# Performance work log

Hardware: AMD Instinct MI355X
Metric: run time of the kernel (lower is better)

The kernel has to match this reference:

```python
import jax, jax.numpy as jnp
import numpy as np

H, W = 40, 128
P = H * W            # image tokens
N = P                # point tokens (matches source where N == Hh*Wh)
C = 128
K = 5                # expand_num
PAD = K // 2
KK = K * K           # 25 neighbors
SPOT = 5             # spot_num
NEG = -1e8


def _l2n(x, axis):
    return x / jnp.clip(jnp.linalg.norm(x, axis=axis, keepdims=True), 1e-12)


def _patches(x, mode, cval=0.0):
    # x: (..., H, W) -> (KK, ..., H, W): KxK sliding windows in F.unfold order
    pw = [(0, 0)] * (x.ndim - 2) + [(PAD, PAD), (PAD, PAD)]
    if mode == 'edge':
        xp = jnp.pad(x, pw, mode='edge')
    else:
        xp = jnp.pad(x, pw, mode='constant', constant_values=cval)
    return jnp.stack([xp[..., i:i + H, j:j + W] for i in range(K) for j in range(K)], 0)


def _knn_idx(pts):
    # (N,3) -> (N,KK) nearest-neighbor indices (self first), as knn_points does
    d2 = jnp.sum((pts[:, None, :] - pts[None, :, :]) ** 2, -1)  # (N,N)
    _, idx = jax.lax.top_k(-d2, KK)
    return idx


def setup_inputs():
    key = jax.random.key(0)
    k1, k2, k3 = jax.random.split(key, 3)
    return {
        'im_feats_h': jax.random.normal(k1, (1, P, C), jnp.float32),
        'pc_feats_h': jax.random.normal(k2, (1, N, C), jnp.float32),
        'points_h': jax.random.normal(k3, (1, N, 3), jnp.float32),
    }


def _forward(imf, pcf, nb):
    # imf: (P,C) image features, pcf: (N,C) point features, nb: (N,KK) point knn
    # --- im_similarity_scores ---
    fmap = imf.T.reshape(C, H, W)
    pat = _patches(fmap, 'edge')                                 # (KK,C,H,W)
    sim = jnp.sum(_l2n(pat, 1) * _l2n(fmap, 0)[None], 1)         # (KK,H,W)
    sim_score = jax.nn.softmax(sim, axis=0)
    # --- pairwise_scores im->pc ---
    s = _l2n(imf, -1) @ _l2n(pcf, -1).T                          # (P,N)
    best_score = s.max(-1).reshape(H, W)
    best_index = s.argmax(-1)                                    # (P,)
    # --- im_select_score ---
    conf = _patches(best_score, 'edge')                          # (KK,H,W)
    idxg = jnp.arange(P).reshape(H, W)
    idx_pat = _patches(idxg, 'const', -1).reshape(KK, P)         # (KK,P)
    select = jnp.where(idx_pat.reshape(KK, H, W) == -1, NEG, sim_score * conf)
    # --- im_seeding ---
    sel = select.at[KK // 2].set(NEG).reshape(KK, P).T           # (P,KK)
    _, tki = jax.lax.top_k(sel, SPOT - 1)
    tki = jnp.concatenate([jnp.full((P, 1), KK // 2, tki.dtype), tki], 1)  # (P,SPOT)
    nb_pix = jnp.clip(jnp.take_along_axis(idx_pat.T, tki, 1), 0, P - 1)
    seed = best_index[nb_pix]                                    # (P,SPOT) pc idx
    # --- im_spoting: expand seeds by point knn, scatter mask, topk-reduce ---
    spot = nb[seed].reshape(P, SPOT * KK)                        # (P,125)
    m = jnp.zeros((P, N), jnp.float32).at[jnp.arange(P)[:, None], spot].set(1.0)
    spot_mask, spot_idx_redu = jax.lax.top_k(m, SPOT * KK)
    # --- pc_similarity_scores ---
    sim_pc = jax.nn.softmax(
        jnp.sum(_l2n(pcf, -1)[:, None] * _l2n(pcf[nb], -1), -1), -1)  # (N,KK)
    # --- pc branch (symmetric, source truncated) ---
    s2 = _l2n(pcf, -1) @ _l2n(imf, -1).T                         # (N,P)
    best_pc_score = s2.max(-1)
    best_pc_idx = s2.argmax(-1)
    select_pc = (sim_pc * best_pc_score[nb]).at[:, 0].set(NEG)   # exclude self
    _, tkp = jax.lax.top_k(select_pc, SPOT - 1)
    tkp = jnp.concatenate([jnp.zeros((N, 1), tkp.dtype), tkp], 1)
    pc_seed = best_pc_idx[jnp.take_along_axis(nb, tkp, 1)]       # (N,SPOT) pixel idx
    # --- pc_spoting: expand seeds in a KxK pixel window ---
    off = jnp.arange(-PAD, PAD + 1)
    r = jnp.clip(pc_seed[..., None, None] // W + off[:, None], 0, H - 1)
    c = jnp.clip(pc_seed[..., None, None] % W + off[None, :], 0, W - 1)
    spot2 = (r * W + c).reshape(N, SPOT * KK)                    # (N,125)
    m2 = jnp.zeros((N, P), jnp.float32).at[jnp.arange(N)[:, None], spot2].set(1.0)
    spot_mask_pc, spot_idx_redu_pc = jax.lax.top_k(m2, SPOT * KK)
    return (select[None], spot_mask[None], spot_idx_redu[None],
            spot_idx_redu_pc[None], spot_mask_pc[None])


def reference(im_feats_h, pc_feats_h, points_h):
    nb = _knn_idx(points_h[0])
    return _forward(im_feats_h[0], pc_feats_h[0], nb)
```

## Files before the change

kernel.cpp:

```cpp
#include <hip/hip_runtime.h>
#include <hip/hip_fp16.h>
#include <float.h>
#include <math.h>

#define HH 40
#define WW 128
#define PP 5120
#define NN 5120
#define CC 128
#define KK 25
#define SPOT 5
#define NEGV -1e8f

#define CSPL 8
#define NSEG 16
#define EPS  1e-4f
#define LOSC 2048.0f
#define RSEGS 16
#define RSEGL (NN / RSEGS)
#define NRMB ((PP + NN) / 4)

typedef _Float16 half8 __attribute__((ext_vector_type(8)));
typedef float f32x4 __attribute__((ext_vector_type(4)));

__global__ __launch_bounds__(256) void k_prep(const float* __restrict__ imf,
                                              const float* __restrict__ pcf,
                                              const float* __restrict__ pts,
                                              float* __restrict__ imn, float* __restrict__ pcn,
                                              __half* __restrict__ imh, __half* __restrict__ iml,
                                              __half* __restrict__ pch, __half* __restrict__ pcl,
                                              int* __restrict__ nb, int* __restrict__ cnt) {
    __shared__ int hist[256];
    __shared__ int wsum2[2][4];
    __shared__ int wsum[4];
    __shared__ int wmin[4];
    __shared__ int s_b, s_need, s_cntLess;
    __shared__ unsigned long long sel[32];
    int t = threadIdx.x;
    int wid = t >> 6, lane = t & 63;

    if (blockIdx.x < NRMB) {
        if (blockIdx.x == 0 && t < 4) cnt[t] = 0;
        int row = blockIdx.x * 4 + wid;
        const float* src; float* dst; __half* dh; __half* dl; int r;
        if (row < PP) { src = imf; dst = imn; dh = imh; dl = iml; r = row; }
        else          { src = pcf; dst = pcn; dh = pch; dl = pcl; r = row - PP; }
        float2 v = *(const float2*)&src[r * CC + lane * 2];
        double ss = (double)v.x * (double)v.x + (double)v.y * (double)v.y;
#pragma unroll
        for (int o = 32; o; o >>= 1) ss += __shfl_xor(ss, o);
        double inv = 1.0 / fmax(sqrt(ss), 1e-12);
        float2 o2 = make_float2((float)((double)v.x * inv), (float)((double)v.y * inv));
        *(float2*)&dst[r * CC + lane * 2] = o2;
        __half hx = __float2half_rn(o2.x), hy = __float2half_rn(o2.y);
        float rx = o2.x - __half2float(hx), ry = o2.y - __half2float(hy);
        __half2 hh; hh.x = hx; hh.y = hy;
        __half2 ll; ll.x = __float2half_rn(rx * LOSC); ll.y = __float2half_rn(ry * LOSC);
        *(__half2*)&dh[r * CC + lane * 2] = hh;
        *(__half2*)&dl[r * CC + lane * 2] = ll;
        return;
    }

    int i = blockIdx.x - NRMB;
    float px = pts[i * 3 + 0], py = pts[i * 3 + 1], pz = pts[i * 3 + 2];

    unsigned k[20];
#pragma unroll
    for (int e = 0; e < 20; ++e) {
        int j = e * 256 + t;
        float dx = __fsub_rn(px, pts[j * 3 + 0]);
        float dy = __fsub_rn(py, pts[j * 3 + 1]);
        float dz = __fsub_rn(pz, pts[j * 3 + 2]);
        float s = __fadd_rn(__fadd_rn(__fmul_rn(dx, dx), __fmul_rn(dy, dy)),
                            __fmul_rn(dz, dz));
        k[e] = __float_as_uint(s);
    }

    int need = KK;
    unsigned bpre = 0;
    for (int bit = 7; bit >= 0; --bit) {
        int c = 0;
        unsigned want = bpre << 1;
#pragma unroll
        for (int e = 0; e < 20; ++e)
            c += ((k[e] >> (24 + bit)) == want);
#pragma unroll
        for (int o = 32; o; o >>= 1) c += __shfl_xor(c, o);
        int par = bit & 1;
        if (lane == 0) wsum2[par][wid] = c;
        __syncthreads();
        int tot = wsum2[par][0] + wsum2[par][1] + wsum2[par][2] + wsum2[par][3];
        if (tot >= need) bpre = want;
        else { bpre = want | 1; need -= tot; }
    }
    unsigned prefix = bpre << 24;

    for (int l = 1; l < 4; ++l) {
        int shift = 24 - 8 * l;
        hist[t] = 0;
        __syncthreads();
        unsigned pmask = 0xFFFFFFFFu << (shift + 8);
#pragma unroll
        for (int e = 0; e < 20; ++e)
            if ((k[e] & pmask) == prefix)
                atomicAdd(&hist[(k[e] >> shift) & 255], 1);
        __syncthreads();
        int v = hist[t], c = v;
#pragma unroll
        for (int o = 1; o < 64; o <<= 1) {
            int u = __shfl_up(c, o);
            if (lane >= o) c += u;
        }
        if (lane == 63) wsum[wid] = c;
        __syncthreads();
        for (int wv = 0; wv < wid; ++wv) c += wsum[wv];
        int cex = c - v;
        if (cex < need && c >= need) { s_b = t; s_need = need - cex; }
        __syncthreads();
        prefix |= ((unsigned)s_b) << shift;
        need = s_need;
        __syncthreads();
    }

    unsigned K = prefix;
    int needK = need;

    if (t == 0) s_cntLess = 0;
    __syncthreads();
#pragma unroll
    for (int e = 0; e < 20; ++e) {
        if (k[e] < K) {
            int slot = atomicAdd(&s_cntLess, 1);
            if (slot < 32)
                sel[slot] = ((unsigned long long)k[e] << 32) | (unsigned)(e * 256 + t);
        }
    }
    __syncthreads();
    int nl = s_cntLess;

    if (t < nl) {
        unsigned long long mine = sel[t];
        int rk = 0;
        for (int s = 0; s < nl; ++s) rk += (sel[s] < mine);
        nb[i * KK + rk] = (int)(mine & 0xFFFFFFFFull);
    }

    unsigned tmask = 0;
#pragma unroll
    for (int e = 0; e < 20; ++e)
        if (k[e] == K) tmask |= 1u << e;

    for (int q = 0; q < needK; ++q) {
        int mi = tmask ? ((__ffs(tmask) - 1) * 256 + t) : 0x7fffffff;
#pragma unroll
        for (int o = 32; o; o >>= 1) mi = min(mi, __shfl_xor(mi, o));
        if (lane == 0) wmin[wid] = mi;
        __syncthreads();
        int g = min(min(wmin[0], wmin[1]), min(wmin[2], wmin[3]));
        if (t == 0) nb[i * KK + nl + q] = g;
        if ((g & 255) == t) tmask &= ~(1u << (g >> 8));
        __syncthreads();
    }
}

__global__ __launch_bounds__(256) void k_rowmax(const __half* __restrict__ imh,
                                                const __half* __restrict__ iml,
                                                const __half* __restrict__ pch,
                                                const __half* __restrict__ pcl,
                                                float* __restrict__ pval,
                                                float* __restrict__ pv2,
                                                int* __restrict__ pidx) {
    const __half* Ah = (blockIdx.z == 0) ? imh : pch;
    const __half* Al = (blockIdx.z == 0) ? iml : pcl;
    const __half* Bh = (blockIdx.z == 0) ? pch : imh;
    const __half* Bl = (blockIdx.z == 0) ? pcl : iml;
    __shared__ char sB[2 * 16384];

    int t = threadIdx.x;
    int wave = t >> 6, l = t & 63;
    int wrow = wave >> 1, wcol = wave & 1;
    int lg = l >> 4, lc = l & 15;
    int rb = blockIdx.x * 64;
    const int segLen = NN / CSPL;
    const int nCh = segLen / 32;
    int segbase = blockIdx.y * segLen;
    int srow = l >> 4;
    int sblk = l & 15;

    half8 Afh[2][4], Afl[2][4];
#pragma unroll
    for (int rt = 0; rt < 2; ++rt)
#pragma unroll
        for (int ks = 0; ks < 4; ++ks) {
            int row = rb + wrow * 32 + rt * 16 + lc;
            int ho = ks * 32 + lg * 8;
            Afh[rt][ks] = *(const half8*)&Ah[(size_t)row * CC + ho];
            Afl[rt][ks] = *(const half8*)&Al[(size_t)row * CC + ho];
        }

    float v1[2][4], v2[2][4]; int i1[2][4];
#pragma unroll
    for (int rt = 0; rt < 2; ++rt)
#pragma unroll
        for (int rg = 0; rg < 4; ++rg) { v1[rt][rg] = -1e30f; v2[rt][rg] = -1e30f; i1[rt][rg] = 0; }

    auto stage = [&](int bufsel, int chbase) {
#pragma unroll
        for (int b = 0; b < 2; ++b) {
            int rbase = wave * 8 + b * 4;
            int r = rbase + srow;
            int gblk = sblk ^ (r & 7);
            __builtin_amdgcn_global_load_lds(
                (const __attribute__((address_space(1))) void*)
                    &Bh[(size_t)(chbase + r) * CC + gblk * 8],
                (__attribute__((address_space(3))) void*)
                    (sB + bufsel * 16384 + rbase * 256),
                16, 0, 0);
            __builtin_amdgcn_global_load_lds(
                (const __attribute__((address_space(1))) void*)
                    &Bl[(size_t)(chbase + r) * CC + gblk * 8],
                (__attribute__((address_space(3))) void*)
                    (sB + bufsel * 16384 + 8192 + rbase * 256),
                16, 0, 0);
        }
    };

    stage(0, segbase);
    __syncthreads();

    int cur = 0;
    for (int c = 0; c < nCh; ++c) {
        if (c + 1 < nCh) stage(cur ^ 1, segbase + (c + 1) * 32);

        f32x4 aH[2], aX[2];
#pragma unroll
        for (int rt = 0; rt < 2; ++rt) {
            aH[rt] = (f32x4){0.f, 0.f, 0.f, 0.f};
            aX[rt] = (f32x4){0.f, 0.f, 0.f, 0.f};
        }

        const char* bufp = sB + cur * 16384;
#pragma unroll
        for (int ks = 0; ks < 4; ++ks) {
            int kb = ks * 64 + lg * 16;
            int row = wcol * 16 + lc;
            int off = row * 256 + (kb ^ ((row & 7) << 4));
            half8 bh = *(const half8*)(bufp + off);
            half8 bl = *(const half8*)(bufp + 8192 + off);
#pragma unroll
            for (int rt = 0; rt < 2; ++rt) {
                aH[rt] = __builtin_amdgcn_mfma_f32_16x16x32_f16(
                    Afh[rt][ks], bh, aH[rt], 0, 0, 0);
                aX[rt] = __builtin_amdgcn_mfma_f32_16x16x32_f16(
                    Afh[rt][ks], bl, aX[rt], 0, 0, 0);
                aX[rt] = __builtin_amdgcn_mfma_f32_16x16x32_f16(
                    Afl[rt][ks], bh, aX[rt], 0, 0, 0);
            }
        }

#pragma unroll
        for (int rt = 0; rt < 2; ++rt) {
            int col = segbase + c * 32 + wcol * 16 + lc;
#pragma unroll
            for (int rg = 0; rg < 4; ++rg) {
                float v = aH[rt][rg] + aX[rt][rg] * (1.0f / LOSC);
                bool gt = v > v1[rt][rg];
                v2[rt][rg] = gt ? v1[rt][rg] : fmaxf(v2[rt][rg], v);
                i1[rt][rg] = gt ? col : i1[rt][rg];
                v1[rt][rg] = gt ? v : v1[rt][rg];
            }
        }
        __syncthreads();
        cur ^= 1;
    }

#pragma unroll
    for (int rt = 0; rt < 2; ++rt)
#pragma unroll
        for (int rg = 0; rg < 4; ++rg) {
            float a1 = v1[rt][rg], a2 = v2[rt][rg]; int ai = i1[rt][rg];
#pragma unroll
            for (int o = 1; o < 16; o <<= 1) {
                float o1 = __shfl_xor(a1, o);
                float o2v = __shfl_xor(a2, o);
                int   oi = __shfl_xor(ai, o);
                if (o1 > a1) { a2 = fmaxf(a1, o2v); a1 = o1; ai = oi; }
                else         { a2 = fmaxf(a2, o1); }
            }
            if (lc == 0) {
                int seg = blockIdx.y * 2 + wcol;
                size_t o = ((size_t)blockIdx.z * NSEG + seg) * PP
                         + rb + wrow * 32 + rt * 16 + lg * 4 + rg;
                pval[o] = a1; pv2[o] = a2; pidx[o] = ai;
            }
        }
}

__global__ void k_reduce_exact(const float* __restrict__ pval, const float* __restrict__ pv2,
                               const int* __restrict__ pidx,
                               const float* __restrict__ imn, const float* __restrict__ pcn,
                               int* __restrict__ bestI, int* __restrict__ bestPI,
                               double* __restrict__ bestSd, double* __restrict__ bestPSd,
                               int* __restrict__ list2, int* __restrict__ cnt) {
    int wid = threadIdx.x >> 6, lane = threadIdx.x & 63;
    int row = blockIdx.x * 4 + wid;
    int side = (row >= PP) ? 1 : 0;
    int r = side ? (row - PP) : row;
    size_t base = (size_t)side * NSEG * PP + r;

    float v1 = -1e30f, v2 = -1e30f; int i1 = 0x7fffffff;
    if (lane < NSEG) {
        v1 = pval[base + (size_t)lane * PP];
        v2 = pv2[base + (size_t)lane * PP];
        i1 = pidx[base + (size_t)lane * PP];
    }
#pragma unroll
    for (int o = 1; o < 16; o <<= 1) {
        float o1 = __shfl_xor(v1, o);
        float o2v = __shfl_xor(v2, o);
        int   oi = __shfl_xor(i1, o);
        if (o1 > v1) { v2 = fmaxf(v1, o2v); v1 = o1; i1 = oi; }
        else         { v2 = fmaxf(v2, o1); }
    }
    int bi = __shfl(i1, 0);
    float b1 = __shfl(v1, 0), b2 = __shfl(v2, 0);

    const float* A = side ? pcn : imn;
    const float* B = side ? imn : pcn;
    float2 av = *(const float2*)&A[(size_t)r * CC + lane * 2];
    float2 bv = *(const float2*)&B[(size_t)bi * CC + lane * 2];
    double s = (double)av.x * (double)bv.x + (double)av.y * (double)bv.y;
#pragma unroll
    for (int o = 32; o; o >>= 1) s += __shfl_xor(s, o);

    if (lane == 0) {
        if (side == 0) { bestI[r] = bi; bestSd[r] = s; }
        else           { bestPI[r] = bi; bestPSd[r] = s; }
        if (b1 - b2 < EPS) {
            int slot = atomicAdd(&cnt[0], 1);
            list2[slot] = r | (side << 16);
        }
    }
}

__global__ void k_recheck64a(const float* __restrict__ imn, const float* __restrict__ pcn,
                             const int* __restrict__ list2, const int* __restrict__ cnt,
                             double* __restrict__ rqv, int* __restrict__ rqi) {
    __shared__ double ad[CC];
    __shared__ double rv[4];
    __shared__ int    ri[4];
    int seg = blockIdx.x, t = threadIdx.x;
    int wid = t >> 6, lane = t & 63;
    int total = cnt[0];
    for (int e = blockIdx.y; e < total; e += gridDim.y) {
        __syncthreads();
        int ent = list2[e];
        int r = ent & 0xffff, side = ent >> 16;
        const float* Arow = (side == 0 ? imn : pcn) + (size_t)r * CC;
        const float* B    = (side == 0 ? pcn : imn);
        if (t < CC) ad[t] = (double)Arow[t];
        __syncthreads();
        double bv = -1e300; int bi = 0x7fffffff;
        for (int j = seg * RSEGL + t; j < (seg + 1) * RSEGL; j += 256) {
            double s0 = 0.0, s1 = 0.0, s2 = 0.0, s3 = 0.0;
#pragma unroll 8
            for (int c4 = 0; c4 < CC / 4; ++c4) {
                float4 b = *(const float4*)&B[(size_t)j * CC + c4 * 4];
                s0 += ad[c4 * 4 + 0] * (double)b.x;
                s1 += ad[c4 * 4 + 1] * (double)b.y;
                s2 += ad[c4 * 4 + 2] * (double)b.z;
                s3 += ad[c4 * 4 + 3] * (double)b.w;
            }
            double s = (s0 + s1) + (s2 + s3);
            if (s > bv || (s == bv && j < bi)) { bv = s; bi = j; }
        }
#pragma unroll
        for (int o = 32; o; o >>= 1) {
            double ov = __shfl_xor(bv, o); int oi = __shfl_xor(bi, o);
            if (ov > bv || (ov == bv && oi < bi)) { bv = ov; bi = oi; }
        }
        if (lane == 0) { rv[wid] = bv; ri[wid] = bi; }
        __syncthreads();
        if (t == 0) {
            for (int wv = 1; wv < 4; ++wv)
                if (rv[wv] > bv || (rv[wv] == bv && ri[wv] < bi)) { bv = rv[wv]; bi = ri[wv]; }
            rqv[(size_t)e * RSEGS + seg] = bv;
            rqi[(size_t)e * RSEGS + seg] = bi;
        }
        __syncthreads();
    }
}

__global__ void k_recheck64b(const int* __restrict__ list2, const int* __restrict__ cnt,
                             const double* __restrict__ rqv, const int* __restrict__ rqi,
                             double* __restrict__ bestSd, int* __restrict__ bestI,
                             double* __restrict__ bestPSd, int* __restrict__ bestPI) {
    int e = blockIdx.x * 256 + threadIdx.x;
    if (e >= cnt[0]) return;
    double bv = rqv[(size_t)e * RSEGS]; int bi = rqi[(size_t)e * RSEGS];
#pragma unroll 4
    for (int s = 1; s < RSEGS; ++s) {
        double ov = rqv[(size_t)e * RSEGS + s]; int oi = rqi[(size_t)e * RSEGS + s];
        if (ov > bv || (ov == bv && oi < bi)) { bv = ov; bi = oi; }
    }
    int ent = list2[e];
    int r = ent & 0xffff, side = ent >> 16;
    if (side == 0) { bestSd[r] = bv; bestI[r] = bi; }
    else           { bestPSd[r] = bv; bestPI[r] = bi; }
}

__device__ __forceinline__ void compact_bits_par(const unsigned* bits,
                                                 float* __restrict__ sm,
                                                 float* __restrict__ si, int lane) {
    unsigned w0 = bits[lane];
    unsigned w1 = bits[64 + lane];
    unsigned w2 = (lane < 32) ? bits[128 + lane] : 0u;
    int c0 = __popc(w0), c1 = __popc(w1), c2 = __popc(w2);
    int s0 = c0, s1 = c1, s2 = c2;
#pragma unroll
    for (int o = 1; o < 64; o <<= 1) {
        int u0 = __shfl_up(s0, o); if (lane >= o) s0 += u0;
        int u1 = __shfl_up(s1, o); if (lane >= o) s1 += u1;
        int u2 = __shfl_up(s2, o); if (lane >= o) s2 += u2;
    }
    int tot0 = __shfl(s0, 63);
    int tot1 = __shfl(s1, 63);
    int tot2 = __shfl(s2, 31);
    int nl = tot0 + tot1 + tot2;
    int e0 = s0 - c0;
    int e1 = tot0 + (s1 - c1);
    int e2 = tot0 + tot1 + (s2 - c2);

    {
        int base = e0; unsigned word = w0; int wi = lane;
        while (word) { int pos = __ffs(word) - 1;
            si[base] = (float)(wi * 32 + pos); sm[base] = 1.0f; word &= word - 1; ++base; }
        base = e1; word = w1; wi = 64 + lane;
        while (word) { int pos = __ffs(word) - 1;
            si[base] = (float)(wi * 32 + pos); sm[base] = 1.0f; word &= word - 1; ++base; }
        if (lane < 32) {
            base = e2; word = w2; wi = 128 + lane;
            while (word) { int pos = __ffs(word) - 1;
                si[base] = (float)(wi * 32 + pos); sm[base] = 1.0f; word &= word - 1; ++base; }
        }
    }
    {
        int wi = lane; int base = nl + 32 * wi - e0; unsigned word = ~w0;
        while (word && base < 125) { int pos = __ffs(word) - 1;
            si[base] = (float)(wi * 32 + pos); sm[base] = 0.0f; word &= word - 1; ++base; }
        wi = 64 + lane; base = nl + 32 * wi - e1; word = ~w1;
        while (word && base < 125) { int pos = __ffs(word) - 1;
            si[base] = (float)(wi * 32 + pos); sm[base] = 0.0f; word &= word - 1; ++base; }
        if (lane < 32) {
            wi = 128 + lane; base = nl + 32 * wi - e2; word = ~w2;
            while (word && base < 125) { int pos = __ffs(word) - 1;
                si[base] = (float)(wi * 32 + pos); sm[base] = 0.0f; word &= word - 1; ++base; }
        }
    }
}

__global__ void k_select_spot(const float* __restrict__ imn, const float* __restrict__ pcn,
                              const int* __restrict__ nb,
                              const double* __restrict__ bestSd, const int* __restrict__ bestI,
                              const double* __restrict__ bestPSd, const int* __restrict__ bestPI,
                              float* __restrict__ outSelect,
                              float* __restrict__ outMask, float* __restrict__ outIdx,
                              float* __restrict__ outMaskPc, float* __restrict__ outIdxPc) {
    __shared__ unsigned bits[4][160];
    __shared__ float smv[4][125];
    __shared__ float siv[4][125];
    int t = threadIdx.x;
    int wid = t >> 6, lane = t & 63;
    int bid = blockIdx.x;

    if (bid < PP / 4) {
        int pb = (bid & 7) * (PP / 4 / 8) + (bid >> 3);
        int p = pb * 4 + wid;
        int h = p >> 7, w = p & 127;

        double mysim = -1e300;
        if (lane < KK) {
            int di = lane / 5 - 2, dj = lane % 5 - 2;
            int hc = min(max(h + di, 0), HH - 1);
            int wc = min(max(w + dj, 0), WW - 1);
            const float* crow = &imn[(size_t)p * CC];
            const float* nrow = &imn[(size_t)(hc * WW + wc) * CC];
            double s0 = 0.0, s1 = 0.0, s2 = 0.0, s3 = 0.0;
#pragma unroll 8
            for (int c = 0; c < CC; c += 4) {
                float4 cv = *(const float4*)&crow[c];
                float4 nv = *(const float4*)&nrow[c];
                s0 += (double)cv.x * (double)nv.x;
                s1 += (double)cv.y * (double)nv.y;
                s2 += (double)cv.z * (double)nv.z;
                s3 += (double)cv.w * (double)nv.w;
            }
            mysim = (s0 + s1) + (s2 + s3);
        }
        double mx = mysim;
#pragma unroll
        for (int o = 1; o < 64; o <<= 1) mx = fmax(mx, __shfl_xor(mx, o));

        double e = 0.0;
        if (lane < KK) e = exp(mysim - mx);
        double sum = e;
#pragma unroll
        for (int o = 32; o; o >>= 1) sum += __shfl_xor(sum, o);
        double inv = 1.0 / sum;

        double selv = -1e300;
        if (lane < KK) {
            int di = lane / 5 - 2, dj = lane % 5 - 2;
            int h2 = h + di, w2 = w + dj;
            bool valid = (h2 >= 0 && h2 < HH && w2 >= 0 && w2 < WW);
            int hc = min(max(h2, 0), HH - 1), wc = min(max(w2, 0), WW - 1);
            double conf = bestSd[hc * WW + wc];
            double so = valid ? (e * inv * conf) : (double)NEGV;
            outSelect[lane * PP + p] = (float)so;
            selv = (lane == 12) ? (double)NEGV : so;
        }

        int tks[5]; tks[0] = 12;
        double sv = selv; int sk = (lane < KK) ? lane : 63;
#pragma unroll
        for (int s = 0; s < 4; ++s) {
            double bv = sv; int bk = sk;
#pragma unroll
            for (int o = 1; o < 64; o <<= 1) {
                double ov = __shfl_xor(bv, o);
                int ok = __shfl_xor(bk, o);
                if (ov > bv || (ov == bv && ok < bk)) { bv = ov; bk = ok; }
            }
            tks[s + 1] = bk;
            if (sk == bk) sv = -1e300;
        }

        int sd0, sd1, sd2, sd3, sd4;
#pragma unroll
        for (int s = 0; s < 5; ++s) {
            int k = tks[s];
            int di = k / 5 - 2, dj = k % 5 - 2;
            int h2 = h + di, w2 = w + dj;
            int pix = (h2 >= 0 && h2 < HH && w2 >= 0 && w2 < WW) ? (h2 * WW + w2) : -1;
            pix = min(max(pix, 0), PP - 1);
            int sd = bestI[pix];
            if (s == 0) sd0 = sd; else if (s == 1) sd1 = sd;
            else if (s == 2) sd2 = sd; else if (s == 3) sd3 = sd; else sd4 = sd;
        }

        for (int w2 = lane; w2 < 160; w2 += 64) bits[wid][w2] = 0u;
        __syncthreads();
        for (int e2 = lane; e2 < 125; e2 += 64) {
            int q = e2 / 25;
            int sd = (q == 0) ? sd0 : (q == 1) ? sd1 : (q == 2) ? sd2 : (q == 3) ? sd3 : sd4;
            int pt = nb[sd * KK + (e2 % 25)];
            atomicOr(&bits[wid][pt >> 5], 1u << (pt & 31));
        }
        __syncthreads();
        compact_bits_par(bits[wid], smv[wid], siv[wid], lane);
        for (int e2 = lane; e2 < 125; e2 += 64) {
            outMask[p * 125 + e2] = smv[wid][e2];
            outIdx[p * 125 + e2]  = siv[wid][e2];
        }
    } else {
        int bid2 = bid - PP / 4;
        int ib = (bid2 & 7) * (PP / 4 / 8) + (bid2 >> 3);
        int i = ib * 4 + wid;

        double mysim = -1e300;
        if (lane < KK) {
            int nbs = nb[i * KK + lane];
            const float* crow = &pcn[(size_t)i * CC];
            const float* nrow = &pcn[(size_t)nbs * CC];
            double s0 = 0.0, s1 = 0.0, s2 = 0.0, s3 = 0.0;
#pragma unroll 8
            for (int c = 0; c < CC; c += 4) {
                float4 cv = *(const float4*)&crow[c];
                float4 nv = *(const float4*)&nrow[c];
                s0 += (double)cv.x * (double)nv.x;
                s1 += (double)cv.y * (double)nv.y;
                s2 += (double)cv.z * (double)nv.z;
                s3 += (double)cv.w * (double)nv.w;
            }
            mysim = (s0 + s1) + (s2 + s3);
        }
        double mx = mysim;
#pragma unroll
        for (int o = 1; o < 64; o <<= 1) mx = fmax(mx, __shfl_xor(mx, o));

        double e = 0.0;
        if (lane < KK) e = exp(mysim - mx);
        double sum = e;
#pragma unroll
        for (int o = 32; o; o >>= 1) sum += __shfl_xor(sum, o);
        double inv = 1.0 / sum;

        double selv = -1e300;
        if (lane < KK)
            selv = (lane == 0) ? (double)NEGV : (e * inv * bestPSd[nb[i * KK + lane]]);

        int tks[5]; tks[0] = 0;
        double sv = selv; int sk = (lane < KK) ? lane : 63;
#pragma unroll
        for (int s = 0; s < 4; ++s) {
            double bv = sv; int bk = sk;
#pragma unroll
            for (int o = 1; o < 64; o <<= 1) {
                double ov = __shfl_xor(bv, o);
                int ok = __shfl_xor(bk, o);
                if (ov > bv || (ov == bv && ok < bk)) { bv = ov; bk = ok; }
            }
            tks[s + 1] = bk;
            if (sk == bk) sv = -1e300;
        }

        int sd0, sd1, sd2, sd3, sd4;
#pragma unroll
        for (int s = 0; s < 5; ++s) {
            int nbs = nb[i * KK + tks[s]];
            int sd = bestPI[nbs];
            if (s == 0) sd0 = sd; else if (s == 1) sd1 = sd;
            else if (s == 2) sd2 = sd; else if (s == 3) sd3 = sd; else sd4 = sd;
        }

        for (int w2 = lane; w2 < 160; w2 += 64) bits[wid][w2] = 0u;
        __syncthreads();
        for (int e2 = lane; e2 < 125; e2 += 64) {
            int q = e2 / 25;
            int sd = (q == 0) ? sd0 : (q == 1) ? sd1 : (q == 2) ? sd2 : (q == 3) ? sd3 : sd4;
            int kk = e2 % 25;
            int r0 = sd >> 7, c0 = sd & 127;
            int r = min(max(r0 + kk / 5 - 2, 0), HH - 1);
            int c = min(max(c0 + kk % 5 - 2, 0), WW - 1);
            int pix = r * WW + c;
            atomicOr(&bits[wid][pix >> 5], 1u << (pix & 31));
        }
        __syncthreads();
        compact_bits_par(bits[wid], smv[wid], siv[wid], lane);
        for (int e2 = lane; e2 < 125; e2 += 64) {
            outMaskPc[i * 125 + e2] = smv[wid][e2];
            outIdxPc[i * 125 + e2]  = siv[wid][e2];
        }
    }
}

extern "C" void kernel_launch(void* const* d_in, const int* in_sizes, int n_in,
                              void* d_out, int out_size, void* d_ws, size_t ws_size,
                              hipStream_t stream) {
    const float* imf = (const float*)d_in[0];
    const float* pcf = (const float*)d_in[1];
    const float* pts = (const float*)d_in[2];
    float* out = (float*)d_out;

    char* w = (char*)d_ws;
    double* bestSd  = (double*)w;  w += (size_t)PP * 8;
    double* bestPSd = (double*)w;  w += (size_t)NN * 8;
    double* rqv     = (double*)w;  w += (size_t)(PP + NN) * RSEGS * 8;
    float*  imn     = (float*)w;   w += (size_t)PP * CC * 4;
    float*  pcn     = (float*)w;   w += (size_t)NN * CC * 4;
    __half* imh     = (__half*)w;  w += (size_t)PP * CC * 2;
    __half* iml     = (__half*)w;  w += (size_t)PP * CC * 2;
    __half* pch     = (__half*)w;  w += (size_t)NN * CC * 2;
    __half* pcl     = (__half*)w;  w += (size_t)NN * CC * 2;
    float*  pval    = (float*)w;   w += (size_t)2 * NSEG * PP * 4;
    float*  pv2     = (float*)w;   w += (size_t)2 * NSEG * PP * 4;
    int*    pidx    = (int*)w;     w += (size_t)2 * NSEG * PP * 4;
    int*    rqi     = (int*)w;     w += (size_t)(PP + NN) * RSEGS * 4;
    int*    nb      = (int*)w;     w += (size_t)NN * KK * 4;
    int*    bestI   = (int*)w;     w += (size_t)PP * 4;
    int*    bestPI  = (int*)w;     w += (size_t)NN * 4;
    int*    list2   = (int*)w;     w += (size_t)(PP + NN) * 4;
    int*    cnt     = (int*)w;     w += 256;

    float* outSelect = out;
    float* outMask   = out + KK * PP;
    float* outIdx    = outMask + PP * 125;
    float* outIdxPc  = outIdx + PP * 125;
    float* outMaskPc = outIdxPc + NN * 125;

    k_prep<<<NRMB + NN, 256, 0, stream>>>(imf, pcf, pts, imn, pcn,
                                          imh, iml, pch, pcl, nb, cnt);
    k_rowmax<<<dim3(PP / 64, CSPL, 2), 256, 0, stream>>>(imh, iml, pch, pcl,
                                                         pval, pv2, pidx);
    k_reduce_exact<<<(PP + NN) / 4, 256, 0, stream>>>(pval, pv2, pidx, imn, pcn,
                                                      bestI, bestPI, bestSd, bestPSd,
                                                      list2, cnt);
    k_recheck64a<<<dim3(RSEGS, 256), 256, 0, stream>>>(imn, pcn, list2, cnt, rqv, rqi);
    k_recheck64b<<<(PP + NN) / 256, 256, 0, stream>>>(list2, cnt, rqv, rqi,
                                                      bestSd, bestI, bestPSd, bestPI);
    k_select_spot<<<2 * PP / 4, 256, 0, stream>>>(imn, pcn, nb, bestSd, bestI,
                                                  bestPSd, bestPI, outSelect,
                                                  outMask, outIdx, outMaskPc, outIdxPc);
}
```

Before: 171.5 us.

## Fuse KNN selection with rowmax GEMM into one interleaved-block kernel

```diff
diff --git a/kernel.cpp b/kernel.cpp
--- a/kernel.cpp
+++ b/kernel.cpp
@@ -23,45 +23,190 @@
 typedef _Float16 half8 __attribute__((ext_vector_type(8)));
 typedef float f32x4 __attribute__((ext_vector_type(4)));
 
-__global__ __launch_bounds__(256) void k_prep(const float* __restrict__ imf,
+__global__ __launch_bounds__(256) void k_norm(const float* __restrict__ imf,
                                               const float* __restrict__ pcf,
-                                              const float* __restrict__ pts,
                                               float* __restrict__ imn, float* __restrict__ pcn,
                                               __half* __restrict__ imh, __half* __restrict__ iml,
                                               __half* __restrict__ pch, __half* __restrict__ pcl,
-                                              int* __restrict__ nb, int* __restrict__ cnt) {
-    __shared__ int hist[256];
-    __shared__ int wsum2[2][4];
-    __shared__ int wsum[4];
-    __shared__ int wmin[4];
-    __shared__ int s_b, s_need, s_cntLess;
-    __shared__ unsigned long long sel[32];
+                                              int* __restrict__ cnt) {
     int t = threadIdx.x;
     int wid = t >> 6, lane = t & 63;
-
-    if (blockIdx.x < NRMB) {
-        if (blockIdx.x == 0 && t < 4) cnt[t] = 0;
-        int row = blockIdx.x * 4 + wid;
-        const float* src; float* dst; __half* dh; __half* dl; int r;
-        if (row < PP) { src = imf; dst = imn; dh = imh; dl = iml; r = row; }
-        else          { src = pcf; dst = pcn; dh = pch; dl = pcl; r = row - PP; }
-        float2 v = *(const float2*)&src[r * CC + lane * 2];
-        double ss = (double)v.x * (double)v.x + (double)v.y * (double)v.y;
-#pragma unroll
-        for (int o = 32; o; o >>= 1) ss += __shfl_xor(ss, o);
-        double inv = 1.0 / fmax(sqrt(ss), 1e-12);
-        float2 o2 = make_float2((float)((double)v.x * inv), (float)((double)v.y * inv));
-        *(float2*)&dst[r * CC + lane * 2] = o2;
-        __half hx = __float2half_rn(o2.x), hy = __float2half_rn(o2.y);
-        float rx = o2.x - __half2float(hx), ry = o2.y - __half2float(hy);
-        __half2 hh; hh.x = hx; hh.y = hy;
-        __half2 ll; ll.x = __float2half_rn(rx * LOSC); ll.y = __float2half_rn(ry * LOSC);
-        *(__half2*)&dh[r * CC + lane * 2] = hh;
-        *(__half2*)&dl[r * CC + lane * 2] = ll;
+    if (blockIdx.x == 0 && t < 4) cnt[t] = 0;
+    int row = blockIdx.x * 4 + wid;
+    const float* src; float* dst; __half* dh; __half* dl; int r;
+    if (row < PP) { src = imf; dst = imn; dh = imh; dl = iml; r = row; }
+    else          { src = pcf; dst = pcn; dh = pch; dl = pcl; r = row - PP; }
+    float2 v = *(const float2*)&src[r * CC + lane * 2];
+    double ss = (double)v.x * (double)v.x + (double)v.y * (double)v.y;
+#pragma unroll
+    for (int o = 32; o; o >>= 1) ss += __shfl_xor(ss, o);
+    double inv = 1.0 / fmax(sqrt(ss), 1e-12);
+    float2 o2 = make_float2((float)((double)v.x * inv), (float)((double)v.y * inv));
+    *(float2*)&dst[r * CC + lane * 2] = o2;
+    __half hx = __float2half_rn(o2.x), hy = __float2half_rn(o2.y);
+    float rx = o2.x - __half2float(hx), ry = o2.y - __half2float(hy);
+    __half2 hh; hh.x = hx; hh.y = hy;
+    __half2 ll; ll.x = __float2half_rn(rx * LOSC); ll.y = __float2half_rn(ry * LOSC);
+    *(__half2*)&dh[r * CC + lane * 2] = hh;
+    *(__half2*)&dl[r * CC + lane * 2] = ll;
+}
+
+struct KnnShared {
+    unsigned long long sel[32];
+    int hist[256];
+    int wsum2[2][4];
+    int wsum[4];
+    int wmin[4];
+    int s_b, s_need, s_cntLess;
+};
+
+__global__ __launch_bounds__(256) void k_mix(const __half* __restrict__ imh,
+                                             const __half* __restrict__ iml,
+                                             const __half* __restrict__ pch,
+                                             const __half* __restrict__ pcl,
+                                             const float* __restrict__ pts,
+                                             float* __restrict__ pval,
+                                             float* __restrict__ pv2,
+                                             int* __restrict__ pidx,
+                                             int* __restrict__ nb) {
+    __shared__ __align__(16) char smem[2 * 16384];
+    int t = threadIdx.x;
+    int wid = t >> 6, lane = t & 63;
+    int bid = blockIdx.x;
+
+    if (bid % 5 == 0) {
+        int rid = bid / 5;
+        int bx = rid % 80;
+        int by = (rid / 80) % 8;
+        int bz = rid / 640;
+        const __half* Ah = (bz == 0) ? imh : pch;
+        const __half* Al = (bz == 0) ? iml : pcl;
+        const __half* Bh = (bz == 0) ? pch : imh;
+        const __half* Bl = (bz == 0) ? pcl : iml;
+        char* sB = smem;
+
+        int wave = wid, l = lane;
+        int wrow = wave >> 1, wcol = wave & 1;
+        int lg = l >> 4, lc = l & 15;
+        int rb = bx * 64;
+        const int segLen = NN / CSPL;
+        const int nCh = segLen / 32;
+        int segbase = by * segLen;
+        int srow = l >> 4;
+        int sblk = l & 15;
+
+        half8 Afh[2][4], Afl[2][4];
+#pragma unroll
+        for (int rt = 0; rt < 2; ++rt)
+#pragma unroll
+            for (int ks = 0; ks < 4; ++ks) {
+                int row = rb + wrow * 32 + rt * 16 + lc;
+                int ho = ks * 32 + lg * 8;
+                Afh[rt][ks] = *(const half8*)&Ah[(size_t)row * CC + ho];
+                Afl[rt][ks] = *(const half8*)&Al[(size_t)row * CC + ho];
+            }
+
+        float v1[2][4], v2[2][4]; int i1[2][4];
+#pragma unroll
+        for (int rt = 0; rt < 2; ++rt)
+#pragma unroll
+            for (int rg = 0; rg < 4; ++rg) { v1[rt][rg] = -1e30f; v2[rt][rg] = -1e30f; i1[rt][rg] = 0; }
+
+        auto stage = [&](int bufsel, int chbase) {
+#pragma unroll
+            for (int b = 0; b < 2; ++b) {
+                int rbase = wave * 8 + b * 4;
+                int r = rbase + srow;
+                int gblk = sblk ^ (r & 7);
+                __builtin_amdgcn_global_load_lds(
+                    (const __attribute__((address_space(1))) void*)
+                        &Bh[(size_t)(chbase + r) * CC + gblk * 8],
+                    (__attribute__((address_space(3))) void*)
+                        (sB + bufsel * 16384 + rbase * 256),
+                    16, 0, 0);
+                __builtin_amdgcn_global_load_lds(
+                    (const __attribute__((address_space(1))) void*)
+                        &Bl[(size_t)(chbase + r) * CC + gblk * 8],
+                    (__attribute__((address_space(3))) void*)
+                        (sB + bufsel * 16384 + 8192 + rbase * 256),
+                    16, 0, 0);
+            }
+        };
+
+        stage(0, segbase);
+        __syncthreads();
+
+        int cur = 0;
+        for (int c = 0; c < nCh; ++c) {
+            if (c + 1 < nCh) stage(cur ^ 1, segbase + (c + 1) * 32);
+
+            f32x4 aH[2], aX[2];
+#pragma unroll
+            for (int rt = 0; rt < 2; ++rt) {
+                aH[rt] = (f32x4){0.f, 0.f, 0.f, 0.f};
+                aX[rt] = (f32x4){0.f, 0.f, 0.f, 0.f};
+            }
+
+            const char* bufp = sB + cur * 16384;
+#pragma unroll
+            for (int ks = 0; ks < 4; ++ks) {
+                int kb = ks * 64 + lg * 16;
+                int row = wcol * 16 + lc;
+                int off = row * 256 + (kb ^ ((row & 7) << 4));
+                half8 bh = *(const half8*)(bufp + off);
+                half8 bl = *(const half8*)(bufp + 8192 + off);
+#pragma unroll
+                for (int rt = 0; rt < 2; ++rt) {
+                    aH[rt] = __builtin_amdgcn_mfma_f32_16x16x32_f16(
+                        Afh[rt][ks], bh, aH[rt], 0, 0, 0);
+                    aX[rt] = __builtin_amdgcn_mfma_f32_16x16x32_f16(
+                        Afh[rt][ks], bl, aX[rt], 0, 0, 0);
+                    aX[rt] = __builtin_amdgcn_mfma_f32_16x16x32_f16(
+                        Afl[rt][ks], bh, aX[rt], 0, 0, 0);
+                }
+            }
+
+#pragma unroll
+            for (int rt = 0; rt < 2; ++rt) {
+                int col = segbase + c * 32 + wcol * 16 + lc;
+#pragma unroll
+                for (int rg = 0; rg < 4; ++rg) {
+                    float v = aH[rt][rg] + aX[rt][rg] * (1.0f / LOSC);
+                    bool gt = v > v1[rt][rg];
+                    v2[rt][rg] = gt ? v1[rt][rg] : fmaxf(v2[rt][rg], v);
+                    i1[rt][rg] = gt ? col : i1[rt][rg];
+                    v1[rt][rg] = gt ? v : v1[rt][rg];
+                }
+            }
+            __syncthreads();
+            cur ^= 1;
+        }
+
+#pragma unroll
+        for (int rt = 0; rt < 2; ++rt)
+#pragma unroll
+            for (int rg = 0; rg < 4; ++rg) {
+                float a1 = v1[rt][rg], a2 = v2[rt][rg]; int ai = i1[rt][rg];
+#pragma unroll
+                for (int o = 1; o < 16; o <<= 1) {
+                    float o1 = __shfl_xor(a1, o);
+                    float o2v = __shfl_xor(a2, o);
+                    int   oi = __shfl_xor(ai, o);
+                    if (o1 > a1) { a2 = fmaxf(a1, o2v); a1 = o1; ai = oi; }
+                    else         { a2 = fmaxf(a2, o1); }
+                }
+                if (lc == 0) {
+                    int seg = by * 2 + wcol;
+                    size_t o = ((size_t)bz * NSEG + seg) * PP
+                             + rb + wrow * 32 + rt * 16 + lg * 4 + rg;
+                    pval[o] = a1; pv2[o] = a2; pidx[o] = ai;
+                }
+            }
         return;
     }
 
-    int i = blockIdx.x - NRMB;
+    KnnShared* ks = (KnnShared*)smem;
+    int i = bid - 1 - bid / 5;
     float px = pts[i * 3 + 0], py = pts[i * 3 + 1], pz = pts[i * 3 + 2];
 
     unsigned k[20];
@@ -87,61 +232,61 @@
 #pragma unroll
         for (int o = 32; o; o >>= 1) c += __shfl_xor(c, o);
         int par = bit & 1;
-        if (lane == 0) wsum2[par][wid] = c;
-        __syncthreads();
-        int tot = wsum2[par][0] + wsum2[par][1] + wsum2[par][2] + wsum2[par][3];
+        if (lane == 0) ks->wsum2[par][wid] = c;
+        __syncthreads();
+        int tot = ks->wsum2[par][0] + ks->wsum2[par][1] + ks->wsum2[par][2] + ks->wsum2[par][3];
         if (tot >= need) bpre = want;
         else { bpre = want | 1; need -= tot; }
     }
     unsigned prefix = bpre << 24;
 
-    for (int l = 1; l < 4; ++l) {
-        int shift = 24 - 8 * l;
-        hist[t] = 0;
+    for (int l2 = 1; l2 < 4; ++l2) {
+        int shift = 24 - 8 * l2;
+        ks->hist[t] = 0;
         __syncthreads();
         unsigned pmask = 0xFFFFFFFFu << (shift + 8);
 #pragma unroll
         for (int e = 0; e < 20; ++e)
             if ((k[e] & pmask) == prefix)
-                atomicAdd(&hist[(k[e] >> shift) & 255], 1);
-        __syncthreads();
-        int v = hist[t], c = v;
+                atomicAdd(&ks->hist[(k[e] >> shift) & 255], 1);
+        __syncthreads();
+        int v = ks->hist[t], c = v;
 #pragma unroll
         for (int o = 1; o < 64; o <<= 1) {
             int u = __shfl_up(c, o);
             if (lane >= o) c += u;
         }
-        if (lane == 63) wsum[wid] = c;
-        __syncthreads();
-        for (int wv = 0; wv < wid; ++wv) c += wsum[wv];
+        if (lane == 63) ks->wsum[wid] = c;
+        __syncthreads();
+        for (int wv = 0; wv < wid; ++wv) c += ks->wsum[wv];
         int cex = c - v;
-        if (cex < need && c >= need) { s_b = t; s_need = need - cex; }
-        __syncthreads();
-        prefix |= ((unsigned)s_b) << shift;
-        need = s_need;
+        if (cex < need && c >= need) { ks->s_b = t; ks->s_need = need - cex; }
+        __syncthreads();
+        prefix |= ((unsigned)ks->s_b) << shift;
+        need = ks->s_need;
         __syncthreads();
     }
 
     unsigned K = prefix;
     int needK = need;
 
-    if (t == 0) s_cntLess = 0;
+    if (t == 0) ks->s_cntLess = 0;
     __syncthreads();
 #pragma unroll
     for (int e = 0; e < 20; ++e) {
         if (k[e] < K) {
-            int slot = atomicAdd(&s_cntLess, 1);
+            int slot = atomicAdd(&ks->s_cntLess, 1);
             if (slot < 32)
-                sel[slot] = ((unsigned long long)k[e] << 32) | (unsigned)(e * 256 + t);
+                ks->sel[slot] = ((unsigned long long)k[e] << 32) | (unsigned)(e * 256 + t);
         }
     }
     __syncthreads();
-    int nl = s_cntLess;
+    int nl = ks->s_cntLess;
 
     if (t < nl) {
-        unsigned long long mine = sel[t];
+        unsigned long long mine = ks->sel[t];
         int rk = 0;
-        for (int s = 0; s < nl; ++s) rk += (sel[s] < mine);
+        for (int s = 0; s < nl; ++s) rk += (ks->sel[s] < mine);
         nb[i * KK + rk] = (int)(mine & 0xFFFFFFFFull);
     }
 
@@ -154,146 +299,13 @@
         int mi = tmask ? ((__ffs(tmask) - 1) * 256 + t) : 0x7fffffff;
 #pragma unroll
         for (int o = 32; o; o >>= 1) mi = min(mi, __shfl_xor(mi, o));
-        if (lane == 0) wmin[wid] = mi;
-        __syncthreads();
-        int g = min(min(wmin[0], wmin[1]), min(wmin[2], wmin[3]));
+        if (lane == 0) ks->wmin[wid] = mi;
+        __syncthreads();
+        int g = min(min(ks->wmin[0], ks->wmin[1]), min(ks->wmin[2], ks->wmin[3]));
         if (t == 0) nb[i * KK + nl + q] = g;
         if ((g & 255) == t) tmask &= ~(1u << (g >> 8));
         __syncthreads();
     }
-}
-
-__global__ __launch_bounds__(256) void k_rowmax(const __half* __restrict__ imh,
-                                                const __half* __restrict__ iml,
-                                                const __half* __restrict__ pch,
-                                                const __half* __restrict__ pcl,
-                                                float* __restrict__ pval,
-                                                float* __restrict__ pv2,
-                                                int* __restrict__ pidx) {
-    const __half* Ah = (blockIdx.z == 0) ? imh : pch;
-    const __half* Al = (blockIdx.z == 0) ? iml : pcl;
-    const __half* Bh = (blockIdx.z == 0) ? pch : imh;
-    const __half* Bl = (blockIdx.z == 0) ? pcl : iml;
-    __shared__ char sB[2 * 16384];
-
-    int t = threadIdx.x;
-    int wave = t >> 6, l = t & 63;
-    int wrow = wave >> 1, wcol = wave & 1;
-    int lg = l >> 4, lc = l & 15;
-    int rb = blockIdx.x * 64;
-    const int segLen = NN / CSPL;
-    const int nCh = segLen / 32;
-    int segbase = blockIdx.y * segLen;
-    int srow = l >> 4;
-    int sblk = l & 15;
-
-    half8 Afh[2][4], Afl[2][4];
-#pragma unroll
-    for (int rt = 0; rt < 2; ++rt)
-#pragma unroll
-        for (int ks = 0; ks < 4; ++ks) {
-            int row = rb + wrow * 32 + rt * 16 + lc;
-            int ho = ks * 32 + lg * 8;
-            Afh[rt][ks] = *(const half8*)&Ah[(size_t)row * CC + ho];
-            Afl[rt][ks] = *(const half8*)&Al[(size_t)row * CC + ho];
-        }
-
-    float v1[2][4], v2[2][4]; int i1[2][4];
-#pragma unroll
-    for (int rt = 0; rt < 2; ++rt)
-#pragma unroll
-        for (int rg = 0; rg < 4; ++rg) { v1[rt][rg] = -1e30f; v2[rt][rg] = -1e30f; i1[rt][rg] = 0; }
-
-    auto stage = [&](int bufsel, int chbase) {
-#pragma unroll
-        for (int b = 0; b < 2; ++b) {
-            int rbase = wave * 8 + b * 4;
-            int r = rbase + srow;
-            int gblk = sblk ^ (r & 7);
-            __builtin_amdgcn_global_load_lds(
-                (const __attribute__((address_space(1))) void*)
-                    &Bh[(size_t)(chbase + r) * CC + gblk * 8],
-                (__attribute__((address_space(3))) void*)
-                    (sB + bufsel * 16384 + rbase * 256),
-                16, 0, 0);
-            __builtin_amdgcn_global_load_lds(
-                (const __attribute__((address_space(1))) void*)
-                    &Bl[(size_t)(chbase + r) * CC + gblk * 8],
-                (__attribute__((address_space(3))) void*)
-                    (sB + bufsel * 16384 + 8192 + rbase * 256),
-                16, 0, 0);
-        }
-    };
-
-    stage(0, segbase);
-    __syncthreads();
-
-    int cur = 0;
-    for (int c = 0; c < nCh; ++c) {
-        if (c + 1 < nCh) stage(cur ^ 1, segbase + (c + 1) * 32);
-
-        f32x4 aH[2], aX[2];
-#pragma unroll
-        for (int rt = 0; rt < 2; ++rt) {
-            aH[rt] = (f32x4){0.f, 0.f, 0.f, 0.f};
-            aX[rt] = (f32x4){0.f, 0.f, 0.f, 0.f};
-        }
-
-        const char* bufp = sB + cur * 16384;
-#pragma unroll
-        for (int ks = 0; ks < 4; ++ks) {
-            int kb = ks * 64 + lg * 16;
-            int row = wcol * 16 + lc;
-            int off = row * 256 + (kb ^ ((row & 7) << 4));
-            half8 bh = *(const half8*)(bufp + off);
-            half8 bl = *(const half8*)(bufp + 8192 + off);
-#pragma unroll
-            for (int rt = 0; rt < 2; ++rt) {
-                aH[rt] = __builtin_amdgcn_mfma_f32_16x16x32_f16(
-                    Afh[rt][ks], bh, aH[rt], 0, 0, 0);
-                aX[rt] = __builtin_amdgcn_mfma_f32_16x16x32_f16(
-                    Afh[rt][ks], bl, aX[rt], 0, 0, 0);
-                aX[rt] = __builtin_amdgcn_mfma_f32_16x16x32_f16(
-                    Afl[rt][ks], bh, aX[rt], 0, 0, 0);
-            }
-        }
-
-#pragma unroll
-        for (int rt = 0; rt < 2; ++rt) {
-            int col = segbase + c * 32 + wcol * 16 + lc;
-#pragma unroll
-            for (int rg = 0; rg < 4; ++rg) {
-                float v = aH[rt][rg] + aX[rt][rg] * (1.0f / LOSC);
-                bool gt = v > v1[rt][rg];
-                v2[rt][rg] = gt ? v1[rt][rg] : fmaxf(v2[rt][rg], v);
-                i1[rt][rg] = gt ? col : i1[rt][rg];
-                v1[rt][rg] = gt ? v : v1[rt][rg];
-            }
-        }
-        __syncthreads();
-        cur ^= 1;
-    }
-
-#pragma unroll
-    for (int rt = 0; rt < 2; ++rt)
-#pragma unroll
-        for (int rg = 0; rg < 4; ++rg) {
-            float a1 = v1[rt][rg], a2 = v2[rt][rg]; int ai = i1[rt][rg];
-#pragma unroll
-            for (int o = 1; o < 16; o <<= 1) {
-                float o1 = __shfl_xor(a1, o);
-                float o2v = __shfl_xor(a2, o);
-                int   oi = __shfl_xor(ai, o);
-                if (o1 > a1) { a2 = fmaxf(a1, o2v); a1 = o1; ai = oi; }
-                else         { a2 = fmaxf(a2, o1); }
-            }
-            if (lc == 0) {
-                int seg = blockIdx.y * 2 + wcol;
-                size_t o = ((size_t)blockIdx.z * NSEG + seg) * PP
-                         + rb + wrow * 32 + rt * 16 + lg * 4 + rg;
-                pval[o] = a1; pv2[o] = a2; pidx[o] = ai;
-            }
-        }
 }
 
 __global__ void k_reduce_exact(const float* __restrict__ pval, const float* __restrict__ pv2,
@@ -678,10 +690,9 @@
     float* outIdxPc  = outIdx + PP * 125;
     float* outMaskPc = outIdxPc + NN * 125;
 
-    k_prep<<<NRMB + NN, 256, 0, stream>>>(imf, pcf, pts, imn, pcn,
-                                          imh, iml, pch, pcl, nb, cnt);
-    k_rowmax<<<dim3(PP / 64, CSPL, 2), 256, 0, stream>>>(imh, iml, pch, pcl,
-                                                         pval, pv2, pidx);
+    k_norm<<<NRMB, 256, 0, stream>>>(imf, pcf, imn, pcn, imh, iml, pch, pcl, cnt);
+    k_mix<<<1280 + NN, 256, 0, stream>>>(imh, iml, pch, pcl, pts,
+                                         pval, pv2, pidx, nb);
     k_reduce_exact<<<(PP + NN) / 4, 256, 0, stream>>>(pval, pv2, pidx, imn, pcn,
                                                       bestI, bestPI, bestSd, bestPSd,
                                                       list2, cnt);
```

After: 200.1 us. 1.17x slower.

## Compute KNN radix-select per wavefront instead of per block

Applied to the files above, without the earlier changes.

```diff
diff --git a/kernel.cpp b/kernel.cpp
--- a/kernel.cpp
+++ b/kernel.cpp
@@ -30,12 +30,9 @@
                                               __half* __restrict__ imh, __half* __restrict__ iml,
                                               __half* __restrict__ pch, __half* __restrict__ pcl,
                                               int* __restrict__ nb, int* __restrict__ cnt) {
-    __shared__ int hist[256];
-    __shared__ int wsum2[2][4];
-    __shared__ int wsum[4];
-    __shared__ int wmin[4];
-    __shared__ int s_b, s_need, s_cntLess;
-    __shared__ unsigned long long sel[32];
+    __shared__ int hist[4][256];
+    __shared__ unsigned long long sel[4][32];
+    __shared__ int scnt[4];
     int t = threadIdx.x;
     int wid = t >> 6, lane = t & 63;
 
@@ -61,13 +58,13 @@
         return;
     }
 
-    int i = blockIdx.x - NRMB;
+    int i = (blockIdx.x - NRMB) * 4 + wid;
     float px = pts[i * 3 + 0], py = pts[i * 3 + 1], pz = pts[i * 3 + 2];
 
-    unsigned k[20];
-#pragma unroll
-    for (int e = 0; e < 20; ++e) {
-        int j = e * 256 + t;
+    unsigned k[80];
+#pragma unroll
+    for (int e = 0; e < 80; ++e) {
+        int j = e * 64 + lane;
         float dx = __fsub_rn(px, pts[j * 3 + 0]);
         float dy = __fsub_rn(py, pts[j * 3 + 1]);
         float dz = __fsub_rn(pz, pts[j * 3 + 2]);
@@ -79,87 +76,94 @@
     int need = KK;
     unsigned bpre = 0;
     for (int bit = 7; bit >= 0; --bit) {
+        unsigned want = bpre << 1;
         int c = 0;
-        unsigned want = bpre << 1;
-#pragma unroll
-        for (int e = 0; e < 20; ++e)
+#pragma unroll
+        for (int e = 0; e < 80; ++e)
             c += ((k[e] >> (24 + bit)) == want);
 #pragma unroll
         for (int o = 32; o; o >>= 1) c += __shfl_xor(c, o);
-        int par = bit & 1;
-        if (lane == 0) wsum2[par][wid] = c;
-        __syncthreads();
-        int tot = wsum2[par][0] + wsum2[par][1] + wsum2[par][2] + wsum2[par][3];
-        if (tot >= need) bpre = want;
-        else { bpre = want | 1; need -= tot; }
+        if (c >= need) bpre = want;
+        else { bpre = want | 1; need -= c; }
     }
     unsigned prefix = bpre << 24;
 
     for (int l = 1; l < 4; ++l) {
         int shift = 24 - 8 * l;
-        hist[t] = 0;
-        __syncthreads();
+        *(int4*)&hist[wid][lane * 4] = make_int4(0, 0, 0, 0);
         unsigned pmask = 0xFFFFFFFFu << (shift + 8);
 #pragma unroll
-        for (int e = 0; e < 20; ++e)
+        for (int e = 0; e < 80; ++e)
             if ((k[e] & pmask) == prefix)
-                atomicAdd(&hist[(k[e] >> shift) & 255], 1);
-        __syncthreads();
-        int v = hist[t], c = v;
+                atomicAdd(&hist[wid][(k[e] >> shift) & 255], 1);
+        int h0 = hist[wid][lane * 4 + 0];
+        int h1 = hist[wid][lane * 4 + 1];
+        int h2 = hist[wid][lane * 4 + 2];
+        int h3 = hist[wid][lane * 4 + 3];
+        int sum = h0 + h1 + h2 + h3;
+        int inc = sum;
 #pragma unroll
         for (int o = 1; o < 64; o <<= 1) {
-            int u = __shfl_up(c, o);
-            if (lane >= o) c += u;
-        }
-        if (lane == 63) wsum[wid] = c;
-        __syncthreads();
-        for (int wv = 0; wv < wid; ++wv) c += wsum[wv];
-        int cex = c - v;
-        if (cex < need && c >= need) { s_b = t; s_need = need - cex; }
-        __syncthreads();
-        prefix |= ((unsigned)s_b) << shift;
-        need = s_need;
-        __syncthreads();
+            int u = __shfl_up(inc, o);
+            if (lane >= o) inc += u;
+        }
+        int excl = inc - sum;
+        int b = -1, nneed = 0;
+        int c0 = excl + h0;
+        if (excl < need && c0 >= need) { b = lane * 4 + 0; nneed = need - excl; }
+        int c1 = c0 + h1;
+        if (c0 < need && c1 >= need)   { b = lane * 4 + 1; nneed = need - c0; }
+        int c2 = c1 + h2;
+        if (c1 < need && c2 >= need)   { b = lane * 4 + 2; nneed = need - c1; }
+        int c3 = c2 + h3;
+        if (c2 < need && c3 >= need)   { b = lane * 4 + 3; nneed = need - c2; }
+        unsigned long long mf = __ballot(b >= 0);
+        int srcl = __ffsll((long long)mf) - 1;
+        b = __shfl(b, srcl);
+        need = __shfl(nneed, srcl);
+        prefix |= ((unsigned)b) << shift;
     }
 
     unsigned K = prefix;
     int needK = need;
 
-    if (t == 0) s_cntLess = 0;
-    __syncthreads();
-#pragma unroll
-    for (int e = 0; e < 20; ++e) {
+    if (lane == 0) scnt[wid] = 0;
+#pragma unroll
+    for (int e = 0; e < 80; ++e) {
         if (k[e] < K) {
-            int slot = atomicAdd(&s_cntLess, 1);
+            int slot = atomicAdd(&scnt[wid], 1);
             if (slot < 32)
-                sel[slot] = ((unsigned long long)k[e] << 32) | (unsigned)(e * 256 + t);
-        }
-    }
-    __syncthreads();
-    int nl = s_cntLess;
-
-    if (t < nl) {
-        unsigned long long mine = sel[t];
+                sel[wid][slot] = ((unsigned long long)k[e] << 32) | (unsigned)(e * 64 + lane);
+        }
+    }
+    int nl = scnt[wid];
+
+    if (lane < nl) {
+        unsigned long long mine = sel[wid][lane];
         int rk = 0;
-        for (int s = 0; s < nl; ++s) rk += (sel[s] < mine);
+        for (int s = 0; s < nl; ++s) rk += (sel[wid][s] < mine);
         nb[i * KK + rk] = (int)(mine & 0xFFFFFFFFull);
     }
 
-    unsigned tmask = 0;
-#pragma unroll
-    for (int e = 0; e < 20; ++e)
-        if (k[e] == K) tmask |= 1u << e;
+    unsigned long long m0 = 0; unsigned m1 = 0;
+#pragma unroll
+    for (int e = 0; e < 64; ++e)
+        if (k[e] == K) m0 |= 1ull << e;
+#pragma unroll
+    for (int e = 64; e < 80; ++e)
+        if (k[e] == K) m1 |= 1u << (e - 64);
 
     for (int q = 0; q < needK; ++q) {
-        int mi = tmask ? ((__ffs(tmask) - 1) * 256 + t) : 0x7fffffff;
+        int e = m0 ? (__ffsll((long long)m0) - 1) : (m1 ? 64 + __ffs((int)m1) - 1 : -1);
+        int mi = (e >= 0) ? (e * 64 + lane) : 0x7fffffff;
 #pragma unroll
         for (int o = 32; o; o >>= 1) mi = min(mi, __shfl_xor(mi, o));
-        if (lane == 0) wmin[wid] = mi;
-        __syncthreads();
-        int g = min(min(wmin[0], wmin[1]), min(wmin[2], wmin[3]));
-        if (t == 0) nb[i * KK + nl + q] = g;
-        if ((g & 255) == t) tmask &= ~(1u << (g >> 8));
-        __syncthreads();
+        if (lane == 0) nb[i * KK + nl + q] = mi;
+        if ((mi & 63) == lane) {
+            int ge = mi >> 6;
+            if (ge < 64) m0 &= ~(1ull << ge);
+            else         m1 &= ~(1u << (ge - 64));
+        }
     }
 }
 
@@ -678,8 +682,8 @@
     float* outIdxPc  = outIdx + PP * 125;
     float* outMaskPc = outIdxPc + NN * 125;
 
-    k_prep<<<NRMB + NN, 256, 0, stream>>>(imf, pcf, pts, imn, pcn,
-                                          imh, iml, pch, pcl, nb, cnt);
+    k_prep<<<NRMB + NN / 4, 256, 0, stream>>>(imf, pcf, pts, imn, pcn,
+                                              imh, iml, pch, pcl, nb, cnt);
     k_rowmax<<<dim3(PP / 64, CSPL, 2), 256, 0, stream>>>(imh, iml, pch, pcl,
                                                          pval, pv2, pidx);
     k_reduce_exact<<<(PP + NN) / 4, 256, 0, stream>>>(pval, pv2, pidx, imn, pcn,
```

After: 179.8 us. 4.8% more time.
